# Optimization experiments

Measured on AMD Instinct MI355X. Metric: run time of the kernel, lower is better.

The kernel has to match this reference:

```python
import jax, jax.numpy as jnp
import numpy as np

NUM_HEADS = 16
HEAD_DIM = 256
FFN_HIDDEN = 512
NUM_USER_HEADS = 8
EPS = 1e-6
BATCH = 8192


def _make_mask(num_heads, head_dim, num_user_heads):
    m = np.ones((num_heads, head_dim), dtype=np.float32)
    sub = head_dim // num_heads
    m[:num_user_heads, num_user_heads * sub:] = 0.0
    return jnp.asarray(m)


def setup_inputs() -> dict:
    key = jax.random.key(0)
    ks = jax.random.split(key, 6)
    x = jax.random.normal(ks[0], (BATCH, NUM_HEADS, HEAD_DIM), dtype=jnp.float32)
    norm1_w = jnp.ones((HEAD_DIM,), dtype=jnp.float32)
    norm2_w = jnp.ones((HEAD_DIM,), dtype=jnp.float32)
    s_in = 1.0 / np.sqrt(HEAD_DIM)
    s_hid = 1.0 / np.sqrt(FFN_HIDDEN)
    w1 = jax.random.normal(ks[1], (NUM_HEADS, HEAD_DIM, FFN_HIDDEN), dtype=jnp.float32) * s_in
    w3 = jax.random.normal(ks[2], (NUM_HEADS, HEAD_DIM, FFN_HIDDEN), dtype=jnp.float32) * s_in
    w2 = jax.random.normal(ks[3], (NUM_HEADS, FFN_HIDDEN, HEAD_DIM), dtype=jnp.float32) * s_hid
    mask = _make_mask(NUM_HEADS, HEAD_DIM, NUM_USER_HEADS)
    return {"x": x, "norm1_w": norm1_w, "norm2_w": norm2_w,
            "w1": w1, "w3": w3, "w2": w2, "mask": mask}


def _rmsnorm(x, w):
    # x: (B,N,D), w: (D,)
    rms = jax.lax.rsqrt(jnp.mean(x * x, axis=-1, keepdims=True) + EPS)
    return x * rms * w


def _head_mixing(x):
    # Parameter-free cross-head sub-dim exchange:
    # mixed[:, i, j*sub:(j+1)*sub] = x[:, j, i*sub:(i+1)*sub]
    B, N, D = x.shape
    sub = D // N
    return x.reshape(B, N, N, sub).transpose(0, 2, 1, 3).reshape(B, N, D)


def reference(x, norm1_w, norm2_w, w1, w3, w2, mask):
    # UI-decoupled HeadMixing: mask zeroes item-head info flowing into user heads
    mixed = _head_mixing(_rmsnorm(x, norm1_w)) * mask[None, :, :]
    p = mixed + x
    # per-head SwiGLU FFN
    h = _rmsnorm(p, norm2_w)
    a = jnp.einsum('bnd,ndh->bnh', h, w1)  # gate
    b = jnp.einsum('bnd,ndh->bnh', h, w3)  # value
    ffn = jnp.einsum('bnh,nhd->bnd', jax.nn.silu(a) * b, w2)
    return ffn + p
```

## Files before the change

kernel.cpp:

```cpp
#include <hip/hip_runtime.h>
#include <hip/hip_bf16.h>
#include <cstdint>

#define B_SZ 8192
#define NH 16
#define HD 256
#define FH 512
#define BR 64

typedef __bf16 bf16x8 __attribute__((ext_vector_type(8)));
typedef float f32x4 __attribute__((ext_vector_type(4)));

__device__ __forceinline__ void lds_load16(const void* g, void* l) {
  __builtin_amdgcn_global_load_lds(
      (const __attribute__((address_space(1))) unsigned char*)g,
      (__attribute__((address_space(3))) unsigned char*)l, 16, 0, 0);
}

__global__ __launch_bounds__(256) void wcvt_kernel(const float* __restrict__ w1,
                                                   const float* __restrict__ w3,
                                                   const float* __restrict__ w2,
                                                   __bf16* __restrict__ w1t,
                                                   __bf16* __restrict__ w3t,
                                                   __bf16* __restrict__ w2t) {
  int bid = blockIdx.x;
  const float* src;
  __bf16* dst;
  int K, N;
  if (bid < 2048)      { src = w1; dst = w1t; K = 256; N = 512; }
  else if (bid < 4096) { src = w3; dst = w3t; K = 256; N = 512; bid -= 2048; }
  else                 { src = w2; dst = w2t; K = 512; N = 256; bid -= 4096; }
  const int tiles_n = N >> 5, tiles_k = K >> 5;
  const int per_head = tiles_n * tiles_k;
  const int head = bid / per_head;
  const int rem = bid - head * per_head;
  const int tk = rem / tiles_n;
  const int tn = rem - tk * tiles_n;
  __shared__ float tile[32][33];
  const float* s = src + ((size_t)head * K + tk * 32) * N + tn * 32;
  const int r = threadIdx.x >> 3;
  const int c4 = (threadIdx.x & 7) * 4;
  float4 v = *(const float4*)(s + (size_t)r * N + c4);
  tile[r][c4 + 0] = v.x; tile[r][c4 + 1] = v.y;
  tile[r][c4 + 2] = v.z; tile[r][c4 + 3] = v.w;
  __syncthreads();
  __bf16 o[4] __attribute__((aligned(8)));
  #pragma unroll
  for (int j = 0; j < 4; ++j) o[j] = (__bf16)tile[c4 + j][r];
  __bf16* d = dst + ((size_t)head * N + tn * 32 + r) * K + tk * 32 + c4;
  *(uint2*)d = *(uint2*)o;
}

#define PREP_R 8
__global__ __launch_bounds__(256) void prep_kernel(const float* __restrict__ x,
                                                   const float* __restrict__ n1w,
                                                   const float* __restrict__ n2w,
                                                   const float* __restrict__ mask,
                                                   __bf16* __restrict__ p_ws,
                                                   __bf16* __restrict__ h_ws) {
  const int t = threadIdx.x;
  const int g = t >> 4;
  const int li = t & 15;
  __shared__ float xs[16 * 260];
  __shared__ float rms1s[16];

  float n1c[16], n2c[16], mc[16];
  #pragma unroll
  for (int j = 0; j < 4; ++j) {
    *(float4*)(n1c + j * 4) = *(const float4*)(n1w + g * 16 + j * 4);
    *(float4*)(n2c + j * 4) = *(const float4*)(n2w + li * 16 + j * 4);
    *(float4*)(mc + j * 4)  = *(const float4*)(mask + g * HD + li * 16 + j * 4);
  }

  for (int r = 0; r < PREP_R; ++r) {
    const int b = blockIdx.x * PREP_R + r;
    const float* xb = x + (size_t)b * (NH * HD);
    if (r) __syncthreads();

    float xv[16];
    float ss = 0.f;
    #pragma unroll
    for (int j = 0; j < 4; ++j) {
      float4 v = *(const float4*)(xb + g * HD + li * 16 + j * 4);
      *(float4*)(xs + g * 260 + li * 16 + j * 4) = v;
      xv[j * 4 + 0] = v.x; xv[j * 4 + 1] = v.y;
      xv[j * 4 + 2] = v.z; xv[j * 4 + 3] = v.w;
      ss += v.x * v.x + v.y * v.y + v.z * v.z + v.w * v.w;
    }
    #pragma unroll
    for (int d = 1; d < 16; d <<= 1) ss += __shfl_xor(ss, d);
    if (li == 0) rms1s[g] = rsqrtf(ss * (1.f / 256.f) + 1e-6f);
    __syncthreads();

    const float r1 = rms1s[li];
    float pv[16];
    float ss2 = 0.f;
    #pragma unroll
    for (int j = 0; j < 4; ++j) {
      float4 sv = *(const float4*)(xs + li * 260 + g * 16 + j * 4);
      float s4[4] = {sv.x, sv.y, sv.z, sv.w};
      #pragma unroll
      for (int q = 0; q < 4; ++q) {
        const int k = j * 4 + q;
        const float mixed = s4[q] * r1 * n1c[k] * mc[k];
        const float p = mixed + xv[k];
        pv[k] = p;
        ss2 += p * p;
      }
    }
    #pragma unroll
    for (int d = 1; d < 16; d <<= 1) ss2 += __shfl_xor(ss2, d);
    const float r2 = rsqrtf(ss2 * (1.f / 256.f) + 1e-6f);

    __bf16 pb[16] __attribute__((aligned(16)));
    __bf16 hv[16] __attribute__((aligned(16)));
    #pragma unroll
    for (int k = 0; k < 16; ++k) {
      pb[k] = (__bf16)pv[k];
      hv[k] = (__bf16)(pv[k] * r2 * n2c[k]);
    }
    __bf16* pp = p_ws + ((size_t)g * B_SZ + b) * HD + li * 16;
    *(uint4*)(pp + 0) = *(uint4*)(pb + 0);
    *(uint4*)(pp + 8) = *(uint4*)(pb + 8);
    __bf16* hp = h_ws + ((size_t)g * B_SZ + b) * HD + li * 16;
    *(uint4*)(hp + 0) = *(uint4*)(hv + 0);
    *(uint4*)(hp + 8) = *(uint4*)(hv + 8);
  }
}

__global__ __launch_bounds__(256) void ffn_kernel(const __bf16* __restrict__ h_ws,
                                                  const __bf16* __restrict__ w1t,
                                                  const __bf16* __restrict__ w3t,
                                                  const __bf16* __restrict__ w2t,
                                                  const __bf16* __restrict__ p_ws,
                                                  float* __restrict__ out) {
  const int bid = blockIdx.x;
  const int head = bid & 15;
  const int stripe = bid >> 4;
  const int r0 = stripe * BR;
  const int t = threadIdx.x;
  const int wv = t >> 6, lane = t & 63;
  const int mlane = lane & 15, quad = lane >> 4;

  __shared__ __bf16 Hs[BR * HD];
  __shared__ __bf16 Wbuf[8192];
  __shared__ __bf16 Sc[BR * 64];

  const __bf16* Hb = h_ws + ((size_t)head * B_SZ + r0) * HD;
  {
    const int rloc = lane >> 5;
    const int ch = lane & 31;
    #pragma unroll
    for (int i = 0; i < 8; ++i) {
      const int row = wv * 16 + i * 2 + rloc;
      const int gch = ch ^ (row & 15);
      lds_load16(Hb + (size_t)row * HD + gch * 8, Hs + (wv * 16 + i * 2) * HD);
    }
  }

  f32x4 oacc[4][4];
  #pragma unroll
  for (int mt = 0; mt < 4; ++mt)
    #pragma unroll
    for (int nt = 0; nt < 4; ++nt) oacc[mt][nt] = (f32x4){0.f, 0.f, 0.f, 0.f};

  const __bf16* W1h = w1t + (size_t)head * FH * HD;
  const __bf16* W3h = w3t + (size_t)head * FH * HD;
  const __bf16* W2h = w2t + (size_t)head * HD * FH;

  __syncthreads();

  for (int hc = 0; hc < 8; ++hc) {
    f32x4 g[4], v[4];
    #pragma unroll
    for (int nt = 0; nt < 4; ++nt) {
      g[nt] = (f32x4){0.f, 0.f, 0.f, 0.f};
      v[nt] = (f32x4){0.f, 0.f, 0.f, 0.f};
    }
    #pragma unroll
    for (int kk = 0; kk < 4; ++kk) {
      __syncthreads();
      {
        const int rl = lane >> 3;
        const int c = lane & 7;
        const int gch = c ^ rl;
        #pragma unroll
        for (int i = 0; i < 2; ++i) {
          const int rb = wv * 16 + i * 8;
          const __bf16* gsrc1 = W1h + (size_t)(hc * 64 + rb + rl) * HD + kk * 64 + gch * 8;
          const __bf16* gsrc3 = W3h + (size_t)(hc * 64 + rb + rl) * HD + kk * 64 + gch * 8;
          lds_load16(gsrc1, Wbuf + rb * 64);
          lds_load16(gsrc3, Wbuf + 4096 + rb * 64);
        }
      }
      __syncthreads();
      #pragma unroll
      for (int ks = 0; ks < 2; ++ks) {
        const int ar = wv * 16 + mlane;
        const int ach = (ks * 4 + quad) ^ (ar & 7);
        bf16x8 a1 = *(const bf16x8*)(Wbuf + ar * 64 + ach * 8);
        bf16x8 a3 = *(const bf16x8*)(Wbuf + 4096 + ar * 64 + ach * 8);
        const int gk = kk * 8 + ks * 4 + quad;
        #pragma unroll
        for (int nt = 0; nt < 4; ++nt) {
          const int row = nt * 16 + mlane;
          bf16x8 b = *(const bf16x8*)(Hs + row * HD + (gk ^ (row & 15)) * 8);
          g[nt] = __builtin_amdgcn_mfma_f32_16x16x32_bf16(a1, b, g[nt], 0, 0, 0);
          v[nt] = __builtin_amdgcn_mfma_f32_16x16x32_bf16(a3, b, v[nt], 0, 0, 0);
        }
      }
    }

    #pragma unroll
    for (int nt = 0; nt < 4; ++nt) {
      const int row = nt * 16 + mlane;
      __bf16 sv[4] __attribute__((aligned(8)));
      #pragma unroll
      for (int r = 0; r < 4; ++r) {
        const float gg = g[nt][r];
        sv[r] = (__bf16)(gg / (1.f + __expf(-gg)) * v[nt][r]);
      }
      const int boff = wv * 32 + quad * 8;
      const int ph = ((boff >> 4) ^ (row & 7));
      char* dst = (char*)Sc + row * 128 + ph * 16 + (boff & 15);
      *(uint2*)dst = *(uint2*)sv;
    }
    __syncthreads();

    #pragma unroll
    for (int ks = 0; ks < 2; ++ks) {
      {
        const int rl = lane >> 2;
        const int c = lane & 3;
        const int gch = c ^ (rl & 3);
        #pragma unroll
        for (int i = 0; i < 4; ++i) {
          const int rb = wv * 64 + i * 16;
          const __bf16* gsrc = W2h + (size_t)(rb + rl) * FH + hc * 64 + ks * 32 + gch * 8;
          lds_load16(gsrc, Wbuf + rb * 32);
        }
      }
      __syncthreads();
      bf16x8 a2[4], b2[4];
      #pragma unroll
      for (int mt = 0; mt < 4; ++mt) {
        const int r = wv * 64 + mt * 16 + mlane;
        a2[mt] = *(const bf16x8*)(Wbuf + r * 32 + ((quad ^ (r & 3))) * 8);
      }
      #pragma unroll
      for (int nt = 0; nt < 4; ++nt) {
        const int row = nt * 16 + mlane;
        const int ch = (ks * 4 + quad) ^ (row & 7);
        b2[nt] = *(const bf16x8*)(Sc + row * 64 + ch * 8);
      }
      #pragma unroll
      for (int mt = 0; mt < 4; ++mt)
        #pragma unroll
        for (int nt = 0; nt < 4; ++nt)
          oacc[mt][nt] = __builtin_amdgcn_mfma_f32_16x16x32_bf16(a2[mt], b2[nt], oacc[mt][nt], 0, 0, 0);
      __syncthreads();
    }
  }

  const __bf16* Pb = p_ws + ((size_t)head * B_SZ + r0) * HD;
  float* Ob = out + (size_t)r0 * (NH * HD) + head * HD;
  #pragma unroll
  for (int mt = 0; mt < 4; ++mt)
    #pragma unroll
    for (int nt = 0; nt < 4; ++nt) {
      const int row = nt * 16 + mlane;
      const int oc = wv * 64 + mt * 16 + quad * 4;
      __bf16 pv[4] __attribute__((aligned(8)));
      *(uint2*)pv = *(const uint2*)(Pb + (size_t)row * HD + oc);
      float4 o;
      o.x = oacc[mt][nt][0] + (float)pv[0];
      o.y = oacc[mt][nt][1] + (float)pv[1];
      o.z = oacc[mt][nt][2] + (float)pv[2];
      o.w = oacc[mt][nt][3] + (float)pv[3];
      *(float4*)(Ob + (size_t)row * (NH * HD) + oc) = o;
    }
}

extern "C" void kernel_launch(void* const* d_in, const int* in_sizes, int n_in,
                              void* d_out, int out_size, void* d_ws, size_t ws_size,
                              hipStream_t stream) {
  const float* x    = (const float*)d_in[0];
  const float* n1w  = (const float*)d_in[1];
  const float* n2w  = (const float*)d_in[2];
  const float* w1   = (const float*)d_in[3];
  const float* w3   = (const float*)d_in[4];
  const float* w2   = (const float*)d_in[5];
  const float* mask = (const float*)d_in[6];
  float* out = (float*)d_out;

  char* ws = (char*)d_ws;
  __bf16* p_ws = (__bf16*)(ws + 0);
  __bf16* h_ws = (__bf16*)(ws + 67108864);
  __bf16* w1t  = (__bf16*)(ws + 134217728);
  __bf16* w3t  = (__bf16*)(ws + 138412032);
  __bf16* w2t  = (__bf16*)(ws + 142606336);

  wcvt_kernel<<<6144, 256, 0, stream>>>(w1, w3, w2, w1t, w3t, w2t);
  prep_kernel<<<1024, 256, 0, stream>>>(x, n1w, n2w, mask, p_ws, h_ws);
  ffn_kernel<<<2048, 256, 0, stream>>>(h_ws, w1t, w3t, w2t, p_ws, out);
}
```

Baseline: 482.2 us.

## Double-buffer FFN weight tiles with async LDS prefetch and per-wave waits

Replaces the load-barrier-compute pattern in the FFN kernel with a two-slot LDS ring (Wbuf grows to 16K bf16). Each wave prefetches the next W1/W3 or W2 tile into the idle slot while its MFMAs run. Block-wide __syncthreads are mostly replaced by explicit vmcnt/lgkmcnt waits, because each wave only reads the weight rows it loaded itself. It also raises MFMA issue priority with s_setprio and requests two blocks per CU through launch bounds. The aim is to hide global-load latency and cut barrier stalls. The cost is fragile hand-counted waitcnt logic, higher LDS use per block, and a wasted wrap-around prefetch on the final iteration.

```diff
diff --git a/kernel.cpp b/kernel.cpp
--- a/kernel.cpp
+++ b/kernel.cpp
@@ -10,6 +10,10 @@
 
 typedef __bf16 bf16x8 __attribute__((ext_vector_type(8)));
 typedef float f32x4 __attribute__((ext_vector_type(4)));
+
+#define VMCNT(n) asm volatile("s_waitcnt vmcnt(" #n ")" ::: "memory")
+#define LGKM0()  asm volatile("s_waitcnt lgkmcnt(0)" ::: "memory")
+#define MEMFENCE() asm volatile("" ::: "memory")
 
 __device__ __forceinline__ void lds_load16(const void* g, void* l) {
   __builtin_amdgcn_global_load_lds(
@@ -128,12 +132,12 @@
   }
 }
 
-__global__ __launch_bounds__(256) void ffn_kernel(const __bf16* __restrict__ h_ws,
-                                                  const __bf16* __restrict__ w1t,
-                                                  const __bf16* __restrict__ w3t,
-                                                  const __bf16* __restrict__ w2t,
-                                                  const __bf16* __restrict__ p_ws,
-                                                  float* __restrict__ out) {
+__global__ __launch_bounds__(256, 2) void ffn_kernel(const __bf16* __restrict__ h_ws,
+                                                     const __bf16* __restrict__ w1t,
+                                                     const __bf16* __restrict__ w3t,
+                                                     const __bf16* __restrict__ w2t,
+                                                     const __bf16* __restrict__ p_ws,
+                                                     float* __restrict__ out) {
   const int bid = blockIdx.x;
   const int head = bid & 15;
   const int stripe = bid >> 4;
@@ -142,9 +146,33 @@
   const int wv = t >> 6, lane = t & 63;
   const int mlane = lane & 15, quad = lane >> 4;
 
-  __shared__ __bf16 Hs[BR * HD];
-  __shared__ __bf16 Wbuf[8192];
-  __shared__ __bf16 Sc[BR * 64];
+  __shared__ __bf16 __attribute__((aligned(16))) Hs[BR * HD];
+  __shared__ __bf16 __attribute__((aligned(16))) Wbuf[16384];
+  __shared__ __bf16 __attribute__((aligned(16))) Sc[BR * 64];
+
+  const __bf16* W1h = w1t + (size_t)head * FH * HD;
+  const __bf16* W3h = w3t + (size_t)head * FH * HD;
+  const __bf16* W2h = w2t + (size_t)head * HD * FH;
+
+  auto stage1_issue = [&](__bf16* Ws, int hc, int kk) {
+    const int rl = lane >> 3, c = lane & 7, gch = c ^ rl;
+    #pragma unroll
+    for (int i = 0; i < 2; ++i) {
+      const int rb = wv * 16 + i * 8;
+      const size_t go = (size_t)(hc * 64 + rb + rl) * HD + kk * 64 + gch * 8;
+      lds_load16(W1h + go, Ws + rb * 64);
+      lds_load16(W3h + go, Ws + 4096 + rb * 64);
+    }
+  };
+  auto stage2_issue = [&](__bf16* Ws, int hc, int ks) {
+    const int rl = lane >> 2, c = lane & 3, gch = c ^ (rl & 3);
+    #pragma unroll
+    for (int i = 0; i < 4; ++i) {
+      const int rb = wv * 64 + i * 16;
+      lds_load16(W2h + (size_t)(rb + rl) * FH + hc * 64 + ks * 32 + gch * 8,
+                 Ws + (i >> 1) * 4096 + wv * 1024 + (i & 1) * 512);
+    }
+  };
 
   const __bf16* Hb = h_ws + ((size_t)head * B_SZ + r0) * HD;
   {
@@ -157,6 +185,11 @@
       lds_load16(Hb + (size_t)row * HD + gch * 8, Hs + (wv * 16 + i * 2) * HD);
     }
   }
+  MEMFENCE();
+  stage1_issue(Wbuf, 0, 0);
+  stage1_issue(Wbuf + 8192, 0, 1);
+  VMCNT(8);
+  __builtin_amdgcn_s_barrier();
 
   f32x4 oacc[4][4];
   #pragma unroll
@@ -164,12 +197,6 @@
     #pragma unroll
     for (int nt = 0; nt < 4; ++nt) oacc[mt][nt] = (f32x4){0.f, 0.f, 0.f, 0.f};
 
-  const __bf16* W1h = w1t + (size_t)head * FH * HD;
-  const __bf16* W3h = w3t + (size_t)head * FH * HD;
-  const __bf16* W2h = w2t + (size_t)head * HD * FH;
-
-  __syncthreads();
-
   for (int hc = 0; hc < 8; ++hc) {
     f32x4 g[4], v[4];
     #pragma unroll
@@ -179,35 +206,33 @@
     }
     #pragma unroll
     for (int kk = 0; kk < 4; ++kk) {
-      __syncthreads();
-      {
-        const int rl = lane >> 3;
-        const int c = lane & 7;
-        const int gch = c ^ rl;
-        #pragma unroll
-        for (int i = 0; i < 2; ++i) {
-          const int rb = wv * 16 + i * 8;
-          const __bf16* gsrc1 = W1h + (size_t)(hc * 64 + rb + rl) * HD + kk * 64 + gch * 8;
-          const __bf16* gsrc3 = W3h + (size_t)(hc * 64 + rb + rl) * HD + kk * 64 + gch * 8;
-          lds_load16(gsrc1, Wbuf + rb * 64);
-          lds_load16(gsrc3, Wbuf + 4096 + rb * 64);
-        }
-      }
-      __syncthreads();
+      __bf16* Ws = Wbuf + (kk & 1) * 8192;
+      VMCNT(4);
       #pragma unroll
       for (int ks = 0; ks < 2; ++ks) {
         const int ar = wv * 16 + mlane;
         const int ach = (ks * 4 + quad) ^ (ar & 7);
-        bf16x8 a1 = *(const bf16x8*)(Wbuf + ar * 64 + ach * 8);
-        bf16x8 a3 = *(const bf16x8*)(Wbuf + 4096 + ar * 64 + ach * 8);
+        bf16x8 a1 = *(const bf16x8*)(Ws + ar * 64 + ach * 8);
+        bf16x8 a3 = *(const bf16x8*)(Ws + 4096 + ar * 64 + ach * 8);
         const int gk = kk * 8 + ks * 4 + quad;
+        bf16x8 b[4];
         #pragma unroll
         for (int nt = 0; nt < 4; ++nt) {
           const int row = nt * 16 + mlane;
-          bf16x8 b = *(const bf16x8*)(Hs + row * HD + (gk ^ (row & 15)) * 8);
-          g[nt] = __builtin_amdgcn_mfma_f32_16x16x32_bf16(a1, b, g[nt], 0, 0, 0);
-          v[nt] = __builtin_amdgcn_mfma_f32_16x16x32_bf16(a3, b, v[nt], 0, 0, 0);
+          b[nt] = *(const bf16x8*)(Hs + row * HD + (gk ^ (row & 15)) * 8);
         }
+        if (ks == 1) {
+          LGKM0();
+          if (kk < 2) stage1_issue(Ws, hc, kk + 2);
+          else        stage2_issue(Ws, hc, kk - 2);
+        }
+        __builtin_amdgcn_s_setprio(1);
+        #pragma unroll
+        for (int nt = 0; nt < 4; ++nt) {
+          g[nt] = __builtin_amdgcn_mfma_f32_16x16x32_bf16(a1, b[nt], g[nt], 0, 0, 0);
+          v[nt] = __builtin_amdgcn_mfma_f32_16x16x32_bf16(a3, b[nt], v[nt], 0, 0, 0);
+        }
+        __builtin_amdgcn_s_setprio(0);
       }
     }
 
@@ -225,42 +250,38 @@
       char* dst = (char*)Sc + row * 128 + ph * 16 + (boff & 15);
       *(uint2*)dst = *(uint2*)sv;
     }
-    __syncthreads();
-
+    LGKM0();
+    __builtin_amdgcn_s_barrier();
+
+    const int hcn = (hc + 1) & 7;
     #pragma unroll
     for (int ks = 0; ks < 2; ++ks) {
-      {
-        const int rl = lane >> 2;
-        const int c = lane & 3;
-        const int gch = c ^ (rl & 3);
-        #pragma unroll
-        for (int i = 0; i < 4; ++i) {
-          const int rb = wv * 64 + i * 16;
-          const __bf16* gsrc = W2h + (size_t)(rb + rl) * FH + hc * 64 + ks * 32 + gch * 8;
-          lds_load16(gsrc, Wbuf + rb * 32);
-        }
-      }
-      __syncthreads();
+      __bf16* Ws = Wbuf + (ks & 1) * 8192;
+      VMCNT(4);
       bf16x8 a2[4], b2[4];
       #pragma unroll
-      for (int mt = 0; mt < 4; ++mt) {
-        const int r = wv * 64 + mt * 16 + mlane;
-        a2[mt] = *(const bf16x8*)(Wbuf + r * 32 + ((quad ^ (r & 3))) * 8);
-      }
+      for (int mt = 0; mt < 4; ++mt)
+        a2[mt] = *(const bf16x8*)(Ws + (mt >> 1) * 4096 + wv * 1024 + (mt & 1) * 512
+                                  + mlane * 32 + ((quad ^ (mlane & 3))) * 8);
       #pragma unroll
       for (int nt = 0; nt < 4; ++nt) {
         const int row = nt * 16 + mlane;
-        const int ch = (ks * 4 + quad) ^ (row & 7);
-        b2[nt] = *(const bf16x8*)(Sc + row * 64 + ch * 8);
+        b2[nt] = *(const bf16x8*)(Sc + row * 64 + (((ks * 4 + quad) ^ (row & 7))) * 8);
       }
+      LGKM0();
+      stage1_issue(Ws, hcn, ks);
+      if (ks == 1) __builtin_amdgcn_s_barrier();
+      __builtin_amdgcn_s_setprio(1);
       #pragma unroll
       for (int mt = 0; mt < 4; ++mt)
         #pragma unroll
         for (int nt = 0; nt < 4; ++nt)
           oacc[mt][nt] = __builtin_amdgcn_mfma_f32_16x16x32_bf16(a2[mt], b2[nt], oacc[mt][nt], 0, 0, 0);
-      __syncthreads();
+      __builtin_amdgcn_s_setprio(0);
     }
   }
+
+  VMCNT(0);
 
   const __bf16* Pb = p_ws + ((size_t)head * B_SZ + r0) * HD;
   float* Ob = out + (size_t)r0 * (NH * HD) + head * HD;
```

Measured after the change: 432.9 us. 10.2% less time.
